# Kernel optimization log

Hardware: AMD Instinct MI355X
Metric: run time of the kernel (lower is better)

## Reference

```python
import jax, jax.numpy as jnp
import numpy as np

T, B, E, H = 1024, 4, 1024, 16
D = E // H  # head_dim = 64


def rel_shift(x):
    # Transformer-XL relative shift trick (RelativeShift.forward, batch_first=True).
    # x: [BH, Q, P] -> pad one zero column, reshape [BH, P+1, Q], drop first row, reshape back.
    BH, Q, P = x.shape
    zp = jnp.zeros((BH, Q, 1), x.dtype)
    xp = jnp.concatenate([zp, x], axis=2).reshape(BH, P + 1, Q)
    return xp[:, 1:, :].reshape(BH, Q, P)


def setup_inputs() -> dict:
    key = jax.random.key(0)
    ks = jax.random.split(key, 8)
    std = float(np.sqrt(2.0 / (E + E)))
    causal = jnp.triu(jnp.ones((T, T), dtype=bool), k=1)  # True = masked (future positions)
    return {
        "x": jax.random.normal(ks[0], (T, B, E), dtype=jnp.float32),
        "pos": jax.random.normal(ks[1], (T, 1, E), dtype=jnp.float32),
        "in_proj_weight": jax.random.normal(ks[2], (3 * E, E), dtype=jnp.float32) * std,
        "in_proj_bias": jnp.zeros((3 * E,), dtype=jnp.float32),
        "out_proj_weight": jax.random.normal(ks[3], (E, E), dtype=jnp.float32) * std,
        "out_proj_bias": jnp.zeros((E,), dtype=jnp.float32),
        "pos_proj_weight": jax.random.normal(ks[4], (E, E), dtype=jnp.float32) * std,
        "pos_proj_bias": jnp.zeros((E,), dtype=jnp.float32),
        "r_w_bias": jax.random.normal(ks[5], (H, D), dtype=jnp.float32) * 0.02,
        "r_r_bias": jax.random.normal(ks[6], (H, D), dtype=jnp.float32) * 0.02,
        "attn_mask": causal,
    }


def reference(x, pos, in_proj_weight, in_proj_bias, out_proj_weight, out_proj_bias,
              pos_proj_weight, pos_proj_bias, r_w_bias, r_r_bias, attn_mask):
    Tq, Bb, Ee = x.shape
    scale = 1.0 / np.sqrt(D).astype(np.float32)
    # fused QKV projection; layout [T, B, heads, 3, head_dim] matches
    # view(len_q, bsz*heads, 3, head_dim) in the original.
    qkv = (x @ in_proj_weight.T + in_proj_bias).reshape(Tq, Bb, H, 3, D)
    q = qkv[..., 0, :]  # [T,B,H,D]
    k = qkv[..., 1, :]
    v = qkv[..., 2, :]
    # position projection (shared across batch since pos is [T,1,E])
    r_head_k = (pos[:, 0, :] @ pos_proj_weight.T + pos_proj_bias).reshape(Tq, H, D)  # [P,H,D]
    rw_q = q + r_w_bias  # content bias
    rr_q = q + r_r_bias  # position bias
    ac = jnp.einsum('qbhd,kbhd->bhqk', rw_q, k) * scale            # [B,H,Q,K]
    bd = jnp.einsum('qbhd,phd->bhqp', rr_q, r_head_k) * scale      # [B,H,Q,P]
    bd = rel_shift(bd.reshape(Bb * H, Tq, Tq)).reshape(Bb, H, Tq, Tq)[..., :Tq]
    score = ac + bd
    score = jnp.where(attn_mask[None, None, :, :], -jnp.inf, score)
    attn = jax.nn.softmax(score, axis=-1)                          # [B,H,Q,K]
    ctx = jnp.einsum('bhqk,kbhd->qbhd', attn, v).reshape(Tq, Bb, Ee)
    out = ctx @ out_proj_weight.T + out_proj_bias                  # [T,B,E]
    return out, attn
```

## Files before the change

### kernel.cpp

```cpp
#include <hip/hip_runtime.h>
#include <math.h>

#define TQ 1024
#define BBATCH 4
#define EDIM 1024
#define HHEADS 16
#define DHEAD 64

typedef __bf16 bf16x8 __attribute__((ext_vector_type(8)));
typedef __bf16 bf16x4 __attribute__((ext_vector_type(4)));
typedef float  f32x4  __attribute__((ext_vector_type(4)));

#define LDK 40

template<int MODE>
__global__ __launch_bounds__(256) void gemm_mfma_abt(
    const float* __restrict__ A, const float* __restrict__ B,
    const float* __restrict__ bias, float* __restrict__ C,
    int M, int N, int K)
{
    __shared__ __bf16 As[128 * LDK];
    __shared__ __bf16 Bs[128 * LDK];
    const int tid  = threadIdx.x;
    const int lane = tid & 63;
    const int wid  = tid >> 6;
    const int wr   = wid >> 1, wc = wid & 1;
    const int m0 = blockIdx.y * 128, n0 = blockIdx.x * 128;

    f32x4 acc[4][4] = {};

    const int sm0 = tid >> 2;
    const int sm1 = sm0 + 64;
    const int sk  = (tid & 3) << 3;

    const int fr = lane & 15;
    const int kg = (lane >> 4) << 3;

    for (int k0 = 0; k0 < K; k0 += 32) {
        float4 ra0a = *(const float4*)&A[(size_t)(m0 + sm0) * K + k0 + sk];
        float4 ra0b = *(const float4*)&A[(size_t)(m0 + sm0) * K + k0 + sk + 4];
        float4 ra1a = *(const float4*)&A[(size_t)(m0 + sm1) * K + k0 + sk];
        float4 ra1b = *(const float4*)&A[(size_t)(m0 + sm1) * K + k0 + sk + 4];
        float4 rb0a = *(const float4*)&B[(size_t)(n0 + sm0) * K + k0 + sk];
        float4 rb0b = *(const float4*)&B[(size_t)(n0 + sm0) * K + k0 + sk + 4];
        float4 rb1a = *(const float4*)&B[(size_t)(n0 + sm1) * K + k0 + sk];
        float4 rb1b = *(const float4*)&B[(size_t)(n0 + sm1) * K + k0 + sk + 4];

        __syncthreads();

        bf16x8 w;
        w[0]=(__bf16)ra0a.x; w[1]=(__bf16)ra0a.y; w[2]=(__bf16)ra0a.z; w[3]=(__bf16)ra0a.w;
        w[4]=(__bf16)ra0b.x; w[5]=(__bf16)ra0b.y; w[6]=(__bf16)ra0b.z; w[7]=(__bf16)ra0b.w;
        *(bf16x8*)&As[sm0 * LDK + sk] = w;
        w[0]=(__bf16)ra1a.x; w[1]=(__bf16)ra1a.y; w[2]=(__bf16)ra1a.z; w[3]=(__bf16)ra1a.w;
        w[4]=(__bf16)ra1b.x; w[5]=(__bf16)ra1b.y; w[6]=(__bf16)ra1b.z; w[7]=(__bf16)ra1b.w;
        *(bf16x8*)&As[sm1 * LDK + sk] = w;
        w[0]=(__bf16)rb0a.x; w[1]=(__bf16)rb0a.y; w[2]=(__bf16)rb0a.z; w[3]=(__bf16)rb0a.w;
        w[4]=(__bf16)rb0b.x; w[5]=(__bf16)rb0b.y; w[6]=(__bf16)rb0b.z; w[7]=(__bf16)rb0b.w;
        *(bf16x8*)&Bs[sm0 * LDK + sk] = w;
        w[0]=(__bf16)rb1a.x; w[1]=(__bf16)rb1a.y; w[2]=(__bf16)rb1a.z; w[3]=(__bf16)rb1a.w;
        w[4]=(__bf16)rb1b.x; w[5]=(__bf16)rb1b.y; w[6]=(__bf16)rb1b.z; w[7]=(__bf16)rb1b.w;
        *(bf16x8*)&Bs[sm1 * LDK + sk] = w;

        __syncthreads();

        bf16x8 af[4], bfr[4];
        #pragma unroll
        for (int i = 0; i < 4; ++i) {
            af[i]  = *(const bf16x8*)&As[(wr * 64 + i * 16 + fr) * LDK + kg];
            bfr[i] = *(const bf16x8*)&Bs[(wc * 64 + i * 16 + fr) * LDK + kg];
        }
        #pragma unroll
        for (int mi = 0; mi < 4; ++mi)
        #pragma unroll
        for (int ni = 0; ni < 4; ++ni)
            acc[mi][ni] = __builtin_amdgcn_mfma_f32_16x16x32_bf16(
                af[mi], bfr[ni], acc[mi][ni], 0, 0, 0);
    }

    const int fq = lane >> 4;
    #pragma unroll
    for (int mi = 0; mi < 4; ++mi)
    #pragma unroll
    for (int ni = 0; ni < 4; ++ni) {
        int row = m0 + wr * 64 + mi * 16 + fq * 4;
        int col = n0 + wc * 64 + ni * 16 + fr;
        float bv = bias[col];
        #pragma unroll
        for (int j = 0; j < 4; ++j) {
            float v = acc[mi][ni][j] + bv;
            if (MODE == 0) {
                C[(size_t)(row + j) * N + col] = v;
            } else {
                C[(((size_t)(col >> 6) << 10) + (row + j)) * 64 + (col & 63)] = v;
            }
        }
    }
}

__global__ __launch_bounds__(256) void bias_dots_kernel(
    const float* __restrict__ qkv, const float* __restrict__ Rm,
    const float* __restrict__ rwb, const float* __restrict__ rrb,
    float* __restrict__ cK, float* __restrict__ cR)
{
    int id = blockIdx.x * 256 + threadIdx.x;
    if (id < 65536) {
        int bh = id >> 10, k = id & 1023;
        int b = bh >> 4, h = bh & 15;
        const float* p = &qkv[((size_t)k * 4 + b) * 3072 + h * 192 + 64];
        const float* w = &rwb[h << 6];
        float s = 0.f;
        #pragma unroll
        for (int d = 0; d < 64; d += 4) {
            float4 v = *(const float4*)&p[d];
            s += v.x * w[d] + v.y * w[d + 1] + v.z * w[d + 2] + v.w * w[d + 3];
        }
        cK[id] = s;
    } else if (id < 81920) {
        int id2 = id - 65536;
        int h = id2 >> 10, j = id2 & 1023;
        const float* p = &Rm[(((size_t)h << 10) + j) * 64];
        const float* w = &rrb[h << 6];
        float s = 0.f;
        #pragma unroll
        for (int d = 0; d < 64; d += 4) {
            float4 v = *(const float4*)&p[d];
            s += v.x * w[d] + v.y * w[d + 1] + v.z * w[d + 2] + v.w * w[d + 3];
        }
        cR[id2] = s;
    }
}

#define SLD 72

__global__ __launch_bounds__(256) void score_mfma_kernel(
    const float* __restrict__ qkv, const float* __restrict__ Rm,
    const float* __restrict__ cK, const float* __restrict__ cR,
    float* __restrict__ attn)
{
    int t = blockIdx.x;
    int qt = (int)((sqrtf(8.f * t + 1.f) - 1.f) * 0.5f);
    while ((qt + 1) * (qt + 2) / 2 <= t) ++qt;
    while (qt * (qt + 1) / 2 > t) --qt;
    int kt = t - qt * (qt + 1) / 2;

    const int bh = blockIdx.y;
    const int b = bh >> 4, h = bh & 15;
    const int q0 = qt << 6, k0 = kt << 6;
    const int tid = threadIdx.x, lane = tid & 63, wid = tid >> 6;
    const int fr = lane & 15, fq = lane >> 4, kg = fq << 3;
    const int w16 = wid << 4;
    const int base_j = k0 - q0 + 960;

    __shared__ __bf16 Qs[64 * SLD];
    __shared__ __bf16 Ks[64 * SLD];
    __shared__ __bf16 Rs[64 * SLD];
    __shared__ float  BDs[64][68];

    float4 qreg[4], kreg[4], r0reg[4], r1reg[4];
    #pragma unroll
    for (int s = 0; s < 4; ++s) {
        int idx = (s << 8) + tid;
        int r = idx >> 4, dc = (idx & 15) << 2;
        qreg[s] = *(const float4*)&qkv[((size_t)(q0 + r) * 4 + b) * 3072 + h * 192 + dc];
        kreg[s] = *(const float4*)&qkv[((size_t)(k0 + r) * 4 + b) * 3072 + h * 192 + 64 + dc];
        int j0 = base_j + r;       if (j0 > 1023) j0 = 1023;
        int j1 = base_j + 64 + r;  if (j1 > 1023) j1 = 1023;
        r0reg[s] = *(const float4*)&Rm[(((size_t)h << 10) + j0) * 64 + dc];
        r1reg[s] = *(const float4*)&Rm[(((size_t)h << 10) + j1) * 64 + dc];
    }
    #pragma unroll
    for (int s = 0; s < 4; ++s) {
        int idx = (s << 8) + tid;
        int r = idx >> 4, dc = (idx & 15) << 2;
        bf16x4 w;
        w[0]=(__bf16)qreg[s].x; w[1]=(__bf16)qreg[s].y; w[2]=(__bf16)qreg[s].z; w[3]=(__bf16)qreg[s].w;
        *(bf16x4*)&Qs[r * SLD + dc] = w;
        w[0]=(__bf16)kreg[s].x; w[1]=(__bf16)kreg[s].y; w[2]=(__bf16)kreg[s].z; w[3]=(__bf16)kreg[s].w;
        *(bf16x4*)&Ks[r * SLD + dc] = w;
        w[0]=(__bf16)r0reg[s].x; w[1]=(__bf16)r0reg[s].y; w[2]=(__bf16)r0reg[s].z; w[3]=(__bf16)r0reg[s].w;
        *(bf16x4*)&Rs[r * SLD + dc] = w;
    }
    __syncthreads();

    bf16x8 af0 = *(const bf16x8*)&Qs[(w16 + fr) * SLD + kg];
    bf16x8 af1 = *(const bf16x8*)&Qs[(w16 + fr) * SLD + 32 + kg];

    f32x4 aac[4], abd[4];
    const f32x4 zero4 = {0.f, 0.f, 0.f, 0.f};

    #pragma unroll
    for (int ni = 0; ni < 4; ++ni) {
        bf16x8 b0 = *(const bf16x8*)&Ks[(ni * 16 + fr) * SLD + kg];
        bf16x8 b1 = *(const bf16x8*)&Ks[(ni * 16 + fr) * SLD + 32 + kg];
        aac[ni] = __builtin_amdgcn_mfma_f32_16x16x32_bf16(af0, b0, zero4, 0, 0, 0);
        aac[ni] = __builtin_amdgcn_mfma_f32_16x16x32_bf16(af1, b1, aac[ni], 0, 0, 0);
    }
    #pragma unroll
    for (int ni = 0; ni < 4; ++ni) {
        bf16x8 b0 = *(const bf16x8*)&Rs[(ni * 16 + fr) * SLD + kg];
        bf16x8 b1 = *(const bf16x8*)&Rs[(ni * 16 + fr) * SLD + 32 + kg];
        abd[ni] = __builtin_amdgcn_mfma_f32_16x16x32_bf16(af0, b0, zero4, 0, 0, 0);
        abd[ni] = __builtin_amdgcn_mfma_f32_16x16x32_bf16(af1, b1, abd[ni], 0, 0, 0);
    }
    #pragma unroll
    for (int ni = 0; ni < 4; ++ni)
    #pragma unroll
    for (int j = 0; j < 4; ++j)
        BDs[w16 + fq * 4 + j][ni * 16 + fr] = abd[ni][j];
    asm volatile("s_waitcnt lgkmcnt(0)" ::: "memory");
    #pragma unroll
    for (int ni = 0; ni < 4; ++ni)
    #pragma unroll
    for (int j = 0; j < 4; ++j) {
        int lrow = w16 + fq * 4 + j;
        int widx = (ni * 16 + fr) - lrow + 63;
        if (widx < 64) aac[ni][j] += BDs[lrow][widx];
    }
    __syncthreads();

    #pragma unroll
    for (int s = 0; s < 4; ++s) {
        int idx = (s << 8) + tid;
        int r = idx >> 4, dc = (idx & 15) << 2;
        bf16x4 w;
        w[0]=(__bf16)r1reg[s].x; w[1]=(__bf16)r1reg[s].y; w[2]=(__bf16)r1reg[s].z; w[3]=(__bf16)r1reg[s].w;
        *(bf16x4*)&Rs[r * SLD + dc] = w;
    }
    __syncthreads();

    #pragma unroll
    for (int ni = 0; ni < 4; ++ni) {
        bf16x8 b0 = *(const bf16x8*)&Rs[(ni * 16 + fr) * SLD + kg];
        bf16x8 b1 = *(const bf16x8*)&Rs[(ni * 16 + fr) * SLD + 32 + kg];
        abd[ni] = __builtin_amdgcn_mfma_f32_16x16x32_bf16(af0, b0, zero4, 0, 0, 0);
        abd[ni] = __builtin_amdgcn_mfma_f32_16x16x32_bf16(af1, b1, abd[ni], 0, 0, 0);
    }
    #pragma unroll
    for (int ni = 0; ni < 4; ++ni)
    #pragma unroll
    for (int j = 0; j < 4; ++j)
        BDs[w16 + fq * 4 + j][ni * 16 + fr] = abd[ni][j];
    asm volatile("s_waitcnt lgkmcnt(0)" ::: "memory");
    #pragma unroll
    for (int ni = 0; ni < 4; ++ni)
    #pragma unroll
    for (int j = 0; j < 4; ++j) {
        int lrow = w16 + fq * 4 + j;
        int widx = (ni * 16 + fr) - lrow + 63;
        if (widx >= 64) aac[ni][j] += BDs[lrow][widx - 64];
    }

    #pragma unroll
    for (int ni = 0; ni < 4; ++ni) {
        int lcol = ni * 16 + fr;
        int k = k0 + lcol;
        float ckv = cK[(bh << 10) + k];
        #pragma unroll
        for (int j = 0; j < 4; ++j) {
            int lrow = w16 + fq * 4 + j;
            int q = q0 + lrow;
            int widx = lcol - lrow + 63;
            int jidx = base_j + widx; if (jidx > 1023) jidx = 1023;
            float crv = cR[(h << 10) + jidx];
            float v = 0.125f * (aac[ni][j] + ckv + crv);
            attn[((((size_t)bh << 10) + q) << 10) + k] = v;
        }
    }
}

__global__ __launch_bounds__(256) void softmax_kernel(float* __restrict__ attn)
{
    const int q = blockIdx.x, bh = blockIdx.y;
    float* row = attn + ((((size_t)bh << 10) + q) << 10);
    const int tid = threadIdx.x;
    float4 v = *(const float4*)&row[tid << 2];
    float s[4] = {v.x, v.y, v.z, v.w};
    #pragma unroll
    for (int c = 0; c < 4; ++c)
        if (((tid << 2) + c) > q) s[c] = -INFINITY;

    float m = fmaxf(fmaxf(s[0], s[1]), fmaxf(s[2], s[3]));
    #pragma unroll
    for (int off = 32; off > 0; off >>= 1)
        m = fmaxf(m, __shfl_xor(m, off));
    __shared__ float redm[4];
    __shared__ float reds[4];
    const int lane = tid & 63, wid = tid >> 6;
    if (lane == 0) redm[wid] = m;
    __syncthreads();
    m = fmaxf(fmaxf(redm[0], redm[1]), fmaxf(redm[2], redm[3]));

    float e[4];
    float t = 0.f;
    #pragma unroll
    for (int c = 0; c < 4; ++c) { e[c] = expf(s[c] - m); t += e[c]; }
    #pragma unroll
    for (int off = 32; off > 0; off >>= 1)
        t += __shfl_xor(t, off);
    if (lane == 0) reds[wid] = t;
    __syncthreads();
    t = reds[0] + reds[1] + reds[2] + reds[3];
    float inv = 1.0f / t;
    float4 o;
    o.x = e[0] * inv; o.y = e[1] * inv; o.z = e[2] * inv; o.w = e[3] * inv;
    *(float4*)&row[tid << 2] = o;
}

__global__ __launch_bounds__(256) void ctx_kernel(
    const float* __restrict__ attn, const float* __restrict__ qkv,
    float* __restrict__ ctx)
{
    const int qt = blockIdx.x, bh = blockIdx.y;
    const int b = bh >> 4, h = bh & 15;
    const int q0 = qt << 6;
    const int tid = threadIdx.x, tx = tid & 15, ty = tid >> 4;
    __shared__ __align__(16) float At[64][68];
    __shared__ __align__(16) float Vs[64][68];
    float acc[4][4] = {};

    for (int k0 = 0; k0 <= q0; k0 += 64) {
        #pragma unroll
        for (int s = 0; s < 4; ++s) {
            int idx = s * 256 + tid;
            int r = idx >> 4, cc = (idx & 15) << 2;
            *(float4*)&At[r][cc] =
                *(const float4*)&attn[((((size_t)bh << 10) + q0 + r) << 10) + k0 + cc];
            *(float4*)&Vs[r][cc] =
                *(const float4*)&qkv[((size_t)(k0 + r) * 4 + b) * 3072 + h * 192 + 128 + cc];
        }
        __syncthreads();
        #pragma unroll
        for (int kk = 0; kk < 64; ++kk) {
            float a[4];
            #pragma unroll
            for (int i = 0; i < 4; ++i) a[i] = At[(ty << 2) + i][kk];
            float4 vv = *(const float4*)&Vs[kk][tx << 2];
            float vb[4] = {vv.x, vv.y, vv.z, vv.w};
            #pragma unroll
            for (int i = 0; i < 4; ++i)
            #pragma unroll
            for (int j = 0; j < 4; ++j)
                acc[i][j] += a[i] * vb[j];
        }
        __syncthreads();
    }

    #pragma unroll
    for (int i = 0; i < 4; ++i) {
        int q = q0 + (ty << 2) + i;
        float4 o;
        o.x = acc[i][0]; o.y = acc[i][1]; o.z = acc[i][2]; o.w = acc[i][3];
        *(float4*)&ctx[((size_t)q * 4 + b) * 1024 + (h << 6) + (tx << 2)] = o;
    }
}

extern "C" void kernel_launch(void* const* d_in, const int* in_sizes, int n_in,
                              void* d_out, int out_size, void* d_ws, size_t ws_size,
                              hipStream_t stream)
{
    (void)in_sizes; (void)n_in; (void)out_size; (void)ws_size;
    const float* x     = (const float*)d_in[0];
    const float* pos   = (const float*)d_in[1];
    const float* w_in  = (const float*)d_in[2];
    const float* b_in  = (const float*)d_in[3];
    const float* w_out = (const float*)d_in[4];
    const float* b_out = (const float*)d_in[5];
    const float* w_pos = (const float*)d_in[6];
    const float* b_pos = (const float*)d_in[7];
    const float* rwb   = (const float*)d_in[8];
    const float* rrb   = (const float*)d_in[9];

    float* out  = (float*)d_out;
    float* attn = out + (size_t)TQ * BBATCH * EDIM;

    float* ws  = (float*)d_ws;
    float* qkv = ws;
    float* R   = qkv + (size_t)4096 * 3072;
    float* ctx = R + (size_t)HHEADS * TQ * DHEAD;
    float* cK  = ctx;
    float* cR  = ctx + 65536;

    dim3 blk(256, 1, 1);

    gemm_mfma_abt<0><<<dim3(3072 / 128, 4096 / 128), blk, 0, stream>>>(
        x, w_in, b_in, qkv, 4096, 3072, 1024);
    gemm_mfma_abt<1><<<dim3(1024 / 128, 1024 / 128), blk, 0, stream>>>(
        pos, w_pos, b_pos, R, 1024, 1024, 1024);
    bias_dots_kernel<<<dim3(320), blk, 0, stream>>>(qkv, R, rwb, rrb, cK, cR);
    score_mfma_kernel<<<dim3(136, 64), blk, 0, stream>>>(qkv, R, cK, cR, attn);
    softmax_kernel<<<dim3(1024, 64), blk, 0, stream>>>(attn);
    ctx_kernel<<<dim3(16, 64), blk, 0, stream>>>(attn, qkv, ctx);
    gemm_mfma_abt<0><<<dim3(1024 / 128, 4096 / 128), blk, 0, stream>>>(
        ctx, w_out, b_out, out, 4096, 1024, 1024);
}
```

Before: 434.4 us.

## Fuse score, softmax and context into one online-softmax attention kernel

Replaces the separate score, softmax and context kernels with one kernel per (query tile, batch-head). The kernel computes scores with an online max/sum across key tiles and writes the raw scores. It then reads them back to normalize, writes the probabilities, and does P·V with bf16 MFMA instead of scalar FP32 FMAs. The masked upper tiles are zero-filled inside the kernel. This removes two launches and the separate full-matrix softmax pass, and moves ctx onto matrix cores. In exchange the grid shrinks to 1024 blocks, whose work varies with the query tile and is ordered largest first. Attention still makes a write-read-write round trip, and cK/cR scratch now lives in the output buffer.

After: 546.0 us. 25.7% more time.

```diff
diff --git a/kernel.cpp b/kernel.cpp
--- a/kernel.cpp
+++ b/kernel.cpp
@@ -131,228 +131,228 @@
     }
 }
 
-#define SLD 72
-
-__global__ __launch_bounds__(256) void score_mfma_kernel(
+#define FLD 66
+
+__global__ __launch_bounds__(256) void fused_attn_kernel(
     const float* __restrict__ qkv, const float* __restrict__ Rm,
     const float* __restrict__ cK, const float* __restrict__ cR,
-    float* __restrict__ attn)
+    float* __restrict__ attn, float* __restrict__ ctx)
 {
-    int t = blockIdx.x;
-    int qt = (int)((sqrtf(8.f * t + 1.f) - 1.f) * 0.5f);
-    while ((qt + 1) * (qt + 2) / 2 <= t) ++qt;
-    while (qt * (qt + 1) / 2 > t) --qt;
-    int kt = t - qt * (qt + 1) / 2;
-
+    const int qt = 15 - blockIdx.x;
     const int bh = blockIdx.y;
     const int b = bh >> 4, h = bh & 15;
-    const int q0 = qt << 6, k0 = kt << 6;
+    const int q0 = qt << 6;
     const int tid = threadIdx.x, lane = tid & 63, wid = tid >> 6;
     const int fr = lane & 15, fq = lane >> 4, kg = fq << 3;
     const int w16 = wid << 4;
-    const int base_j = k0 - q0 + 960;
-
-    __shared__ __bf16 Qs[64 * SLD];
-    __shared__ __bf16 Ks[64 * SLD];
-    __shared__ __bf16 Rs[64 * SLD];
-    __shared__ float  BDs[64][68];
-
-    float4 qreg[4], kreg[4], r0reg[4], r1reg[4];
+    const int base0 = 960 - q0;
+
+    __shared__ __align__(16) char smem[42752];
+    __bf16* Qs  = (__bf16*)smem;
+    __bf16* Pl  = (__bf16*)smem;
+    float (*BDs)[68] = (float(*)[68])smem;
+    __bf16* Vt  = (__bf16*)(smem + 8448);
+    __bf16* Ks  = (__bf16*)(smem + 17408);
+    __bf16* Rc0 = (__bf16*)(smem + 25856);
+    __bf16* Rc1 = (__bf16*)(smem + 34304);
+
     #pragma unroll
     for (int s = 0; s < 4; ++s) {
-        int idx = (s << 8) + tid;
-        int r = idx >> 4, dc = (idx & 15) << 2;
-        qreg[s] = *(const float4*)&qkv[((size_t)(q0 + r) * 4 + b) * 3072 + h * 192 + dc];
-        kreg[s] = *(const float4*)&qkv[((size_t)(k0 + r) * 4 + b) * 3072 + h * 192 + 64 + dc];
-        int j0 = base_j + r;       if (j0 > 1023) j0 = 1023;
-        int j1 = base_j + 64 + r;  if (j1 > 1023) j1 = 1023;
-        r0reg[s] = *(const float4*)&Rm[(((size_t)h << 10) + j0) * 64 + dc];
-        r1reg[s] = *(const float4*)&Rm[(((size_t)h << 10) + j1) * 64 + dc];
-    }
-    #pragma unroll
-    for (int s = 0; s < 4; ++s) {
-        int idx = (s << 8) + tid;
-        int r = idx >> 4, dc = (idx & 15) << 2;
+        int idx = (s << 8) + tid, r = idx >> 4, dc = (idx & 15) << 2;
+        float4 vq = *(const float4*)&qkv[((size_t)(q0 + r) * 4 + b) * 3072 + h * 192 + dc];
+        float4 vr = *(const float4*)&Rm[(((size_t)h << 10) + base0 + r) * 64 + dc];
         bf16x4 w;
-        w[0]=(__bf16)qreg[s].x; w[1]=(__bf16)qreg[s].y; w[2]=(__bf16)qreg[s].z; w[3]=(__bf16)qreg[s].w;
-        *(bf16x4*)&Qs[r * SLD + dc] = w;
-        w[0]=(__bf16)kreg[s].x; w[1]=(__bf16)kreg[s].y; w[2]=(__bf16)kreg[s].z; w[3]=(__bf16)kreg[s].w;
-        *(bf16x4*)&Ks[r * SLD + dc] = w;
-        w[0]=(__bf16)r0reg[s].x; w[1]=(__bf16)r0reg[s].y; w[2]=(__bf16)r0reg[s].z; w[3]=(__bf16)r0reg[s].w;
-        *(bf16x4*)&Rs[r * SLD + dc] = w;
+        w[0]=(__bf16)vq.x; w[1]=(__bf16)vq.y; w[2]=(__bf16)vq.z; w[3]=(__bf16)vq.w;
+        *(bf16x4*)&Qs[r * FLD + dc] = w;
+        w[0]=(__bf16)vr.x; w[1]=(__bf16)vr.y; w[2]=(__bf16)vr.z; w[3]=(__bf16)vr.w;
+        *(bf16x4*)&Rc0[r * FLD + dc] = w;
     }
     __syncthreads();
-
-    bf16x8 af0 = *(const bf16x8*)&Qs[(w16 + fr) * SLD + kg];
-    bf16x8 af1 = *(const bf16x8*)&Qs[(w16 + fr) * SLD + 32 + kg];
-
-    f32x4 aac[4], abd[4];
-    const f32x4 zero4 = {0.f, 0.f, 0.f, 0.f};
-
-    #pragma unroll
-    for (int ni = 0; ni < 4; ++ni) {
-        bf16x8 b0 = *(const bf16x8*)&Ks[(ni * 16 + fr) * SLD + kg];
-        bf16x8 b1 = *(const bf16x8*)&Ks[(ni * 16 + fr) * SLD + 32 + kg];
-        aac[ni] = __builtin_amdgcn_mfma_f32_16x16x32_bf16(af0, b0, zero4, 0, 0, 0);
-        aac[ni] = __builtin_amdgcn_mfma_f32_16x16x32_bf16(af1, b1, aac[ni], 0, 0, 0);
-    }
-    #pragma unroll
-    for (int ni = 0; ni < 4; ++ni) {
-        bf16x8 b0 = *(const bf16x8*)&Rs[(ni * 16 + fr) * SLD + kg];
-        bf16x8 b1 = *(const bf16x8*)&Rs[(ni * 16 + fr) * SLD + 32 + kg];
-        abd[ni] = __builtin_amdgcn_mfma_f32_16x16x32_bf16(af0, b0, zero4, 0, 0, 0);
-        abd[ni] = __builtin_amdgcn_mfma_f32_16x16x32_bf16(af1, b1, abd[ni], 0, 0, 0);
+    bf16x8 af0 = *(const bf16x8*)&Qs[(w16 + fr) * FLD + kg];
+    bf16x8 af1 = *(const bf16x8*)&Qs[(w16 + fr) * FLD + 32 + kg];
+
+    float mrow[4] = {-1e30f, -1e30f, -1e30f, -1e30f};
+    float srow[4] = {0.f, 0.f, 0.f, 0.f};
+    const f32x4 z4 = {0.f, 0.f, 0.f, 0.f};
+
+    for (int kt = 0; kt <= qt; ++kt) {
+        const int k0 = kt << 6;
+        __bf16* Rh0 = (kt & 1) ? Rc1 : Rc0;
+        __bf16* Rh1 = (kt & 1) ? Rc0 : Rc1;
+
+        float4 kreg[4], rreg[4];
+        #pragma unroll
+        for (int s = 0; s < 4; ++s) {
+            int idx = (s << 8) + tid, r = idx >> 4, dc = (idx & 15) << 2;
+            kreg[s] = *(const float4*)&qkv[((size_t)(k0 + r) * 4 + b) * 3072 + h * 192 + 64 + dc];
+            int j = base0 + k0 + 64 + r; if (j > 1023) j = 1023;
+            rreg[s] = *(const float4*)&Rm[(((size_t)h << 10) + j) * 64 + dc];
+        }
+        __syncthreads();
+        #pragma unroll
+        for (int s = 0; s < 4; ++s) {
+            int idx = (s << 8) + tid, r = idx >> 4, dc = (idx & 15) << 2;
+            bf16x4 w;
+            w[0]=(__bf16)kreg[s].x; w[1]=(__bf16)kreg[s].y; w[2]=(__bf16)kreg[s].z; w[3]=(__bf16)kreg[s].w;
+            *(bf16x4*)&Ks[r * FLD + dc] = w;
+            w[0]=(__bf16)rreg[s].x; w[1]=(__bf16)rreg[s].y; w[2]=(__bf16)rreg[s].z; w[3]=(__bf16)rreg[s].w;
+            *(bf16x4*)&Rh1[r * FLD + dc] = w;
+        }
+        __syncthreads();
+
+        f32x4 aac[4];
+        #pragma unroll
+        for (int ni = 0; ni < 4; ++ni) {
+            bf16x8 b0 = *(const bf16x8*)&Ks[(ni * 16 + fr) * FLD + kg];
+            bf16x8 b1 = *(const bf16x8*)&Ks[(ni * 16 + fr) * FLD + 32 + kg];
+            aac[ni] = __builtin_amdgcn_mfma_f32_16x16x32_bf16(af0, b0, z4, 0, 0, 0);
+            aac[ni] = __builtin_amdgcn_mfma_f32_16x16x32_bf16(af1, b1, aac[ni], 0, 0, 0);
+        }
+        f32x4 abd[4];
+        #pragma unroll
+        for (int ni = 0; ni < 4; ++ni) {
+            bf16x8 b0 = *(const bf16x8*)&Rh0[(ni * 16 + fr) * FLD + kg];
+            bf16x8 b1 = *(const bf16x8*)&Rh0[(ni * 16 + fr) * FLD + 32 + kg];
+            abd[ni] = __builtin_amdgcn_mfma_f32_16x16x32_bf16(af0, b0, z4, 0, 0, 0);
+            abd[ni] = __builtin_amdgcn_mfma_f32_16x16x32_bf16(af1, b1, abd[ni], 0, 0, 0);
+        }
+        #pragma unroll
+        for (int ni = 0; ni < 4; ++ni)
+        #pragma unroll
+        for (int j = 0; j < 4; ++j)
+            BDs[w16 + fq * 4 + j][ni * 16 + fr] = abd[ni][j];
+        asm volatile("s_waitcnt lgkmcnt(0)" ::: "memory");
+        #pragma unroll
+        for (int ni = 0; ni < 4; ++ni)
+        #pragma unroll
+        for (int j = 0; j < 4; ++j) {
+            int lrow = w16 + fq * 4 + j;
+            int widx = (ni * 16 + fr) - lrow + 63;
+            if (widx < 64) aac[ni][j] += BDs[lrow][widx];
+        }
+        #pragma unroll
+        for (int ni = 0; ni < 4; ++ni) {
+            bf16x8 b0 = *(const bf16x8*)&Rh1[(ni * 16 + fr) * FLD + kg];
+            bf16x8 b1 = *(const bf16x8*)&Rh1[(ni * 16 + fr) * FLD + 32 + kg];
+            abd[ni] = __builtin_amdgcn_mfma_f32_16x16x32_bf16(af0, b0, z4, 0, 0, 0);
+            abd[ni] = __builtin_amdgcn_mfma_f32_16x16x32_bf16(af1, b1, abd[ni], 0, 0, 0);
+        }
+        #pragma unroll
+        for (int ni = 0; ni < 4; ++ni)
+        #pragma unroll
+        for (int j = 0; j < 4; ++j)
+            BDs[w16 + fq * 4 + j][ni * 16 + fr] = abd[ni][j];
+        asm volatile("s_waitcnt lgkmcnt(0)" ::: "memory");
+        #pragma unroll
+        for (int ni = 0; ni < 4; ++ni)
+        #pragma unroll
+        for (int j = 0; j < 4; ++j) {
+            int lrow = w16 + fq * 4 + j;
+            int widx = (ni * 16 + fr) - lrow + 63;
+            if (widx >= 64) aac[ni][j] += BDs[lrow][widx - 64];
+        }
+
+        float sc[4][4];
+        #pragma unroll
+        for (int ni = 0; ni < 4; ++ni) {
+            int lcol = ni * 16 + fr, k = k0 + lcol;
+            float ckv = cK[(bh << 10) + k];
+            #pragma unroll
+            for (int j = 0; j < 4; ++j) {
+                int lrow = w16 + fq * 4 + j;
+                int widx = lcol - lrow + 63;
+                int jidx = base0 + k0 + widx; if (jidx > 1023) jidx = 1023;
+                float v = 0.125f * (aac[ni][j] + ckv + cR[(h << 10) + jidx]);
+                if (kt == qt && lcol > lrow) v = -1e30f;
+                sc[ni][j] = v;
+                attn[((size_t)bh << 20) + ((size_t)(q0 + lrow) << 10) + k] = v;
+            }
+        }
+        #pragma unroll
+        for (int j = 0; j < 4; ++j) {
+            float tmax = fmaxf(fmaxf(sc[0][j], sc[1][j]), fmaxf(sc[2][j], sc[3][j]));
+            tmax = fmaxf(tmax, __shfl_xor(tmax, 1));
+            tmax = fmaxf(tmax, __shfl_xor(tmax, 2));
+            tmax = fmaxf(tmax, __shfl_xor(tmax, 4));
+            tmax = fmaxf(tmax, __shfl_xor(tmax, 8));
+            float mnew = fmaxf(mrow[j], tmax);
+            float ps = __expf(sc[0][j] - mnew) + __expf(sc[1][j] - mnew)
+                     + __expf(sc[2][j] - mnew) + __expf(sc[3][j] - mnew);
+            ps += __shfl_xor(ps, 1); ps += __shfl_xor(ps, 2);
+            ps += __shfl_xor(ps, 4); ps += __shfl_xor(ps, 8);
+            srow[j] = srow[j] * __expf(mrow[j] - mnew) + ps;
+            mrow[j] = mnew;
+        }
+    }
+
+    float inv[4];
+    #pragma unroll
+    for (int j = 0; j < 4; ++j) inv[j] = 1.0f / srow[j];
+
+    asm volatile("s_waitcnt vmcnt(0)" ::: "memory");
+    __syncthreads();
+
+    f32x4 apv[4] = {};
+    for (int kt = 0; kt <= qt; ++kt) {
+        const int k0 = kt << 6;
+        float4 vreg[4];
+        #pragma unroll
+        for (int s = 0; s < 4; ++s) {
+            int idx = (s << 8) + tid, r = idx >> 4, dc = (idx & 15) << 2;
+            vreg[s] = *(const float4*)&qkv[((size_t)(k0 + r) * 4 + b) * 3072 + h * 192 + 128 + dc];
+        }
+        float praw[4][4];
+        #pragma unroll
+        for (int ni = 0; ni < 4; ++ni)
+        #pragma unroll
+        for (int j = 0; j < 4; ++j)
+            praw[ni][j] = attn[((size_t)bh << 20) +
+                               ((size_t)(q0 + w16 + fq * 4 + j) << 10) + k0 + ni * 16 + fr];
+        __syncthreads();
+        #pragma unroll
+        for (int s = 0; s < 4; ++s) {
+            int idx = (s << 8) + tid, r = idx >> 4, dc = (idx & 15) << 2;
+            Vt[(dc + 0) * FLD + r] = (__bf16)vreg[s].x;
+            Vt[(dc + 1) * FLD + r] = (__bf16)vreg[s].y;
+            Vt[(dc + 2) * FLD + r] = (__bf16)vreg[s].z;
+            Vt[(dc + 3) * FLD + r] = (__bf16)vreg[s].w;
+        }
+        #pragma unroll
+        for (int ni = 0; ni < 4; ++ni)
+        #pragma unroll
+        for (int j = 0; j < 4; ++j) {
+            float p = __expf(praw[ni][j] - mrow[j]) * inv[j];
+            attn[((size_t)bh << 20) +
+                 ((size_t)(q0 + w16 + fq * 4 + j) << 10) + k0 + ni * 16 + fr] = p;
+            Pl[(w16 + fq * 4 + j) * FLD + ni * 16 + fr] = (__bf16)p;
+        }
+        __syncthreads();
+        bf16x8 pa0 = *(const bf16x8*)&Pl[(w16 + fr) * FLD + kg];
+        bf16x8 pa1 = *(const bf16x8*)&Pl[(w16 + fr) * FLD + 32 + kg];
+        #pragma unroll
+        for (int ni = 0; ni < 4; ++ni) {
+            bf16x8 bv0 = *(const bf16x8*)&Vt[(ni * 16 + fr) * FLD + kg];
+            bf16x8 bv1 = *(const bf16x8*)&Vt[(ni * 16 + fr) * FLD + 32 + kg];
+            apv[ni] = __builtin_amdgcn_mfma_f32_16x16x32_bf16(pa0, bv0, apv[ni], 0, 0, 0);
+            apv[ni] = __builtin_amdgcn_mfma_f32_16x16x32_bf16(pa1, bv1, apv[ni], 0, 0, 0);
+        }
+    }
+
+    for (int kt = qt + 1; kt < 16; ++kt) {
+        const int k0 = kt << 6;
+        #pragma unroll
+        for (int s = 0; s < 4; ++s) {
+            int idx = (s << 8) + tid, r = idx >> 4, c4 = (idx & 15) << 2;
+            float4 z = {0.f, 0.f, 0.f, 0.f};
+            *(float4*)&attn[((size_t)bh << 20) + ((size_t)(q0 + r) << 10) + k0 + c4] = z;
+        }
     }
     #pragma unroll
     for (int ni = 0; ni < 4; ++ni)
     #pragma unroll
     for (int j = 0; j < 4; ++j)
-        BDs[w16 + fq * 4 + j][ni * 16 + fr] = abd[ni][j];
-    asm volatile("s_waitcnt lgkmcnt(0)" ::: "memory");
-    #pragma unroll
-    for (int ni = 0; ni < 4; ++ni)
-    #pragma unroll
-    for (int j = 0; j < 4; ++j) {
-        int lrow = w16 + fq * 4 + j;
-        int widx = (ni * 16 + fr) - lrow + 63;
-        if (widx < 64) aac[ni][j] += BDs[lrow][widx];
-    }
-    __syncthreads();
-
-    #pragma unroll
-    for (int s = 0; s < 4; ++s) {
-        int idx = (s << 8) + tid;
-        int r = idx >> 4, dc = (idx & 15) << 2;
-        bf16x4 w;
-        w[0]=(__bf16)r1reg[s].x; w[1]=(__bf16)r1reg[s].y; w[2]=(__bf16)r1reg[s].z; w[3]=(__bf16)r1reg[s].w;
-        *(bf16x4*)&Rs[r * SLD + dc] = w;
-    }
-    __syncthreads();
-
-    #pragma unroll
-    for (int ni = 0; ni < 4; ++ni) {
-        bf16x8 b0 = *(const bf16x8*)&Rs[(ni * 16 + fr) * SLD + kg];
-        bf16x8 b1 = *(const bf16x8*)&Rs[(ni * 16 + fr) * SLD + 32 + kg];
-        abd[ni] = __builtin_amdgcn_mfma_f32_16x16x32_bf16(af0, b0, zero4, 0, 0, 0);
-        abd[ni] = __builtin_amdgcn_mfma_f32_16x16x32_bf16(af1, b1, abd[ni], 0, 0, 0);
-    }
-    #pragma unroll
-    for (int ni = 0; ni < 4; ++ni)
-    #pragma unroll
-    for (int j = 0; j < 4; ++j)
-        BDs[w16 + fq * 4 + j][ni * 16 + fr] = abd[ni][j];
-    asm volatile("s_waitcnt lgkmcnt(0)" ::: "memory");
-    #pragma unroll
-    for (int ni = 0; ni < 4; ++ni)
-    #pragma unroll
-    for (int j = 0; j < 4; ++j) {
-        int lrow = w16 + fq * 4 + j;
-        int widx = (ni * 16 + fr) - lrow + 63;
-        if (widx >= 64) aac[ni][j] += BDs[lrow][widx - 64];
-    }
-
-    #pragma unroll
-    for (int ni = 0; ni < 4; ++ni) {
-        int lcol = ni * 16 + fr;
-        int k = k0 + lcol;
-        float ckv = cK[(bh << 10) + k];
-        #pragma unroll
-        for (int j = 0; j < 4; ++j) {
-            int lrow = w16 + fq * 4 + j;
-            int q = q0 + lrow;
-            int widx = lcol - lrow + 63;
-            int jidx = base_j + widx; if (jidx > 1023) jidx = 1023;
-            float crv = cR[(h << 10) + jidx];
-            float v = 0.125f * (aac[ni][j] + ckv + crv);
-            attn[((((size_t)bh << 10) + q) << 10) + k] = v;
-        }
-    }
-}
-
-__global__ __launch_bounds__(256) void softmax_kernel(float* __restrict__ attn)
-{
-    const int q = blockIdx.x, bh = blockIdx.y;
-    float* row = attn + ((((size_t)bh << 10) + q) << 10);
-    const int tid = threadIdx.x;
-    float4 v = *(const float4*)&row[tid << 2];
-    float s[4] = {v.x, v.y, v.z, v.w};
-    #pragma unroll
-    for (int c = 0; c < 4; ++c)
-        if (((tid << 2) + c) > q) s[c] = -INFINITY;
-
-    float m = fmaxf(fmaxf(s[0], s[1]), fmaxf(s[2], s[3]));
-    #pragma unroll
-    for (int off = 32; off > 0; off >>= 1)
-        m = fmaxf(m, __shfl_xor(m, off));
-    __shared__ float redm[4];
-    __shared__ float reds[4];
-    const int lane = tid & 63, wid = tid >> 6;
-    if (lane == 0) redm[wid] = m;
-    __syncthreads();
-    m = fmaxf(fmaxf(redm[0], redm[1]), fmaxf(redm[2], redm[3]));
-
-    float e[4];
-    float t = 0.f;
-    #pragma unroll
-    for (int c = 0; c < 4; ++c) { e[c] = expf(s[c] - m); t += e[c]; }
-    #pragma unroll
-    for (int off = 32; off > 0; off >>= 1)
-        t += __shfl_xor(t, off);
-    if (lane == 0) reds[wid] = t;
-    __syncthreads();
-    t = reds[0] + reds[1] + reds[2] + reds[3];
-    float inv = 1.0f / t;
-    float4 o;
-    o.x = e[0] * inv; o.y = e[1] * inv; o.z = e[2] * inv; o.w = e[3] * inv;
-    *(float4*)&row[tid << 2] = o;
-}
-
-__global__ __launch_bounds__(256) void ctx_kernel(
-    const float* __restrict__ attn, const float* __restrict__ qkv,
-    float* __restrict__ ctx)
-{
-    const int qt = blockIdx.x, bh = blockIdx.y;
-    const int b = bh >> 4, h = bh & 15;
-    const int q0 = qt << 6;
-    const int tid = threadIdx.x, tx = tid & 15, ty = tid >> 4;
-    __shared__ __align__(16) float At[64][68];
-    __shared__ __align__(16) float Vs[64][68];
-    float acc[4][4] = {};
-
-    for (int k0 = 0; k0 <= q0; k0 += 64) {
-        #pragma unroll
-        for (int s = 0; s < 4; ++s) {
-            int idx = s * 256 + tid;
-            int r = idx >> 4, cc = (idx & 15) << 2;
-            *(float4*)&At[r][cc] =
-                *(const float4*)&attn[((((size_t)bh << 10) + q0 + r) << 10) + k0 + cc];
-            *(float4*)&Vs[r][cc] =
-                *(const float4*)&qkv[((size_t)(k0 + r) * 4 + b) * 3072 + h * 192 + 128 + cc];
-        }
-        __syncthreads();
-        #pragma unroll
-        for (int kk = 0; kk < 64; ++kk) {
-            float a[4];
-            #pragma unroll
-            for (int i = 0; i < 4; ++i) a[i] = At[(ty << 2) + i][kk];
-            float4 vv = *(const float4*)&Vs[kk][tx << 2];
-            float vb[4] = {vv.x, vv.y, vv.z, vv.w};
-            #pragma unroll
-            for (int i = 0; i < 4; ++i)
-            #pragma unroll
-            for (int j = 0; j < 4; ++j)
-                acc[i][j] += a[i] * vb[j];
-        }
-        __syncthreads();
-    }
-
-    #pragma unroll
-    for (int i = 0; i < 4; ++i) {
-        int q = q0 + (ty << 2) + i;
-        float4 o;
-        o.x = acc[i][0]; o.y = acc[i][1]; o.z = acc[i][2]; o.w = acc[i][3];
-        *(float4*)&ctx[((size_t)q * 4 + b) * 1024 + (h << 6) + (tx << 2)] = o;
-    }
+        ctx[((size_t)(q0 + w16 + fq * 4 + j) * 4 + b) * 1024 + (h << 6) + ni * 16 + fr]
+            = apv[ni][j];
 }
 
 extern "C" void kernel_launch(void* const* d_in, const int* in_sizes, int n_in,
@@ -378,8 +378,8 @@
     float* qkv = ws;
     float* R   = qkv + (size_t)4096 * 3072;
     float* ctx = R + (size_t)HHEADS * TQ * DHEAD;
-    float* cK  = ctx;
-    float* cR  = ctx + 65536;
+    float* cK  = out;
+    float* cR  = out + 65536;
 
     dim3 blk(256, 1, 1);
 
@@ -388,9 +388,7 @@
     gemm_mfma_abt<1><<<dim3(1024 / 128, 1024 / 128), blk, 0, stream>>>(
         pos, w_pos, b_pos, R, 1024, 1024, 1024);
     bias_dots_kernel<<<dim3(320), blk, 0, stream>>>(qkv, R, rwb, rrb, cK, cR);
-    score_mfma_kernel<<<dim3(136, 64), blk, 0, stream>>>(qkv, R, cK, cR, attn);
-    softmax_kernel<<<dim3(1024, 64), blk, 0, stream>>>(attn);
-    ctx_kernel<<<dim3(16, 64), blk, 0, stream>>>(attn, qkv, ctx);
+    fused_attn_kernel<<<dim3(16, 64), blk, 0, stream>>>(qkv, R, cK, cR, attn, ctx);
     gemm_mfma_abt<0><<<dim3(1024 / 128, 4096 / 128), blk, 0, stream>>>(
         ctx, w_out, b_out, out, 4096, 1024, 1024);
 }
```

## Split softmax into row-stats pass and fuse normalization into bf16 MFMA PV kernel

Applied to the files above, without the earlier changes.

Replaces the full-row softmax kernel with a per-row statistics kernel that computes an online max and inverse sum while reading only the causal prefix of each row. The context kernel now applies exp and normalization on the fly, writes normalized probabilities back to attn, zero-fills the masked upper tiles, and computes P·V with bf16 MFMA instead of fp32 FMA. The aim is to cut one full read/write pass over the attention matrix, skip reading masked tiles, and use matrix cores. The cost is bf16 rounding in the context product, and scratch stats are placed in the output buffer before the final GEMM overwrites it.

Result: faster. 371.8 us (-14.4%).

```diff
diff --git a/kernel.cpp b/kernel.cpp
--- a/kernel.cpp
+++ b/kernel.cpp
@@ -264,95 +264,132 @@
             int jidx = base_j + widx; if (jidx > 1023) jidx = 1023;
             float crv = cR[(h << 10) + jidx];
             float v = 0.125f * (aac[ni][j] + ckv + crv);
+            if (kt == qt && lcol > lrow) v = -1e30f;
             attn[((((size_t)bh << 10) + q) << 10) + k] = v;
         }
     }
 }
 
-__global__ __launch_bounds__(256) void softmax_kernel(float* __restrict__ attn)
-{
-    const int q = blockIdx.x, bh = blockIdx.y;
-    float* row = attn + ((((size_t)bh << 10) + q) << 10);
-    const int tid = threadIdx.x;
-    float4 v = *(const float4*)&row[tid << 2];
-    float s[4] = {v.x, v.y, v.z, v.w};
-    #pragma unroll
-    for (int c = 0; c < 4; ++c)
-        if (((tid << 2) + c) > q) s[c] = -INFINITY;
-
-    float m = fmaxf(fmaxf(s[0], s[1]), fmaxf(s[2], s[3]));
-    #pragma unroll
-    for (int off = 32; off > 0; off >>= 1)
-        m = fmaxf(m, __shfl_xor(m, off));
-    __shared__ float redm[4];
-    __shared__ float reds[4];
-    const int lane = tid & 63, wid = tid >> 6;
-    if (lane == 0) redm[wid] = m;
-    __syncthreads();
-    m = fmaxf(fmaxf(redm[0], redm[1]), fmaxf(redm[2], redm[3]));
-
-    float e[4];
-    float t = 0.f;
-    #pragma unroll
-    for (int c = 0; c < 4; ++c) { e[c] = expf(s[c] - m); t += e[c]; }
-    #pragma unroll
-    for (int off = 32; off > 0; off >>= 1)
-        t += __shfl_xor(t, off);
-    if (lane == 0) reds[wid] = t;
-    __syncthreads();
-    t = reds[0] + reds[1] + reds[2] + reds[3];
-    float inv = 1.0f / t;
-    float4 o;
-    o.x = e[0] * inv; o.y = e[1] * inv; o.z = e[2] * inv; o.w = e[3] * inv;
-    *(float4*)&row[tid << 2] = o;
-}
-
-__global__ __launch_bounds__(256) void ctx_kernel(
-    const float* __restrict__ attn, const float* __restrict__ qkv,
-    float* __restrict__ ctx)
-{
-    const int qt = blockIdx.x, bh = blockIdx.y;
+__global__ __launch_bounds__(256) void row_stats_kernel(
+    const float* __restrict__ attn, float2* __restrict__ stats)
+{
+    const int gw = blockIdx.x * 4 + (threadIdx.x >> 6);
+    const int bh = gw >> 10, q = gw & 1023;
+    const int lane = threadIdx.x & 63;
+    const float* row = attn + ((size_t)bh << 20) + ((size_t)q << 10);
+
+    float m = -1e30f, s = 0.f;
+    const int nc = (q >> 8) + 1;
+    for (int c = 0; c < nc; ++c) {
+        int base = (c << 8) + (lane << 2);
+        float4 v = *(const float4*)&row[base];
+        bool c0 = base + 0 <= q, c1 = base + 1 <= q, c2 = base + 2 <= q, c3 = base + 3 <= q;
+        float e0 = c0 ? v.x : -1e30f, e1 = c1 ? v.y : -1e30f;
+        float e2 = c2 ? v.z : -1e30f, e3 = c3 ? v.w : -1e30f;
+        float tm = fmaxf(fmaxf(e0, e1), fmaxf(e2, e3));
+        float mn = fmaxf(m, tm);
+        s *= __expf(m - mn);
+        if (c0) s += __expf(v.x - mn);
+        if (c1) s += __expf(v.y - mn);
+        if (c2) s += __expf(v.z - mn);
+        if (c3) s += __expf(v.w - mn);
+        m = mn;
+    }
+    #pragma unroll
+    for (int off = 1; off < 64; off <<= 1) {
+        float mo = __shfl_xor(m, off), so = __shfl_xor(s, off);
+        float mn = fmaxf(m, mo);
+        s = s * __expf(m - mn) + so * __expf(mo - mn);
+        m = mn;
+    }
+    if (lane == 0) stats[gw] = make_float2(m, 1.0f / s);
+}
+
+#define FLD 66
+
+__global__ __launch_bounds__(256) void ctx_norm_kernel(
+    const float* __restrict__ qkv, const float2* __restrict__ stats,
+    float* __restrict__ attn, float* __restrict__ ctx)
+{
+    const int qt = 15 - blockIdx.x;
+    const int bh = blockIdx.y;
     const int b = bh >> 4, h = bh & 15;
     const int q0 = qt << 6;
-    const int tid = threadIdx.x, tx = tid & 15, ty = tid >> 4;
-    __shared__ __align__(16) float At[64][68];
-    __shared__ __align__(16) float Vs[64][68];
-    float acc[4][4] = {};
-
-    for (int k0 = 0; k0 <= q0; k0 += 64) {
+    const int tid = threadIdx.x, lane = tid & 63, wid = tid >> 6;
+    const int fr = lane & 15, fq = lane >> 4, kg = fq << 3;
+    const int w16 = wid << 4;
+
+    __shared__ __bf16 Pl[64 * FLD];
+    __shared__ __bf16 Vt[64 * FLD];
+
+    float mrow[4], inv[4];
+    #pragma unroll
+    for (int j = 0; j < 4; ++j) {
+        float2 st = stats[(bh << 10) + q0 + w16 + fq * 4 + j];
+        mrow[j] = st.x; inv[j] = st.y;
+    }
+
+    f32x4 apv[4] = {};
+    for (int kt = 0; kt <= qt; ++kt) {
+        const int k0 = kt << 6;
+        float4 vreg[4];
         #pragma unroll
         for (int s = 0; s < 4; ++s) {
-            int idx = s * 256 + tid;
-            int r = idx >> 4, cc = (idx & 15) << 2;
-            *(float4*)&At[r][cc] =
-                *(const float4*)&attn[((((size_t)bh << 10) + q0 + r) << 10) + k0 + cc];
-            *(float4*)&Vs[r][cc] =
-                *(const float4*)&qkv[((size_t)(k0 + r) * 4 + b) * 3072 + h * 192 + 128 + cc];
-        }
+            int idx = (s << 8) + tid, r = idx >> 4, dc = (idx & 15) << 2;
+            vreg[s] = *(const float4*)&qkv[((size_t)(k0 + r) * 4 + b) * 3072 + h * 192 + 128 + dc];
+        }
+        float praw[4][4];
+        #pragma unroll
+        for (int ni = 0; ni < 4; ++ni)
+        #pragma unroll
+        for (int j = 0; j < 4; ++j)
+            praw[ni][j] = attn[((size_t)bh << 20) +
+                               ((size_t)(q0 + w16 + fq * 4 + j) << 10) + k0 + ni * 16 + fr];
         __syncthreads();
         #pragma unroll
-        for (int kk = 0; kk < 64; ++kk) {
-            float a[4];
-            #pragma unroll
-            for (int i = 0; i < 4; ++i) a[i] = At[(ty << 2) + i][kk];
-            float4 vv = *(const float4*)&Vs[kk][tx << 2];
-            float vb[4] = {vv.x, vv.y, vv.z, vv.w};
-            #pragma unroll
-            for (int i = 0; i < 4; ++i)
-            #pragma unroll
-            for (int j = 0; j < 4; ++j)
-                acc[i][j] += a[i] * vb[j];
+        for (int s = 0; s < 4; ++s) {
+            int idx = (s << 8) + tid, r = idx >> 4, dc = (idx & 15) << 2;
+            Vt[(dc + 0) * FLD + r] = (__bf16)vreg[s].x;
+            Vt[(dc + 1) * FLD + r] = (__bf16)vreg[s].y;
+            Vt[(dc + 2) * FLD + r] = (__bf16)vreg[s].z;
+            Vt[(dc + 3) * FLD + r] = (__bf16)vreg[s].w;
+        }
+        #pragma unroll
+        for (int ni = 0; ni < 4; ++ni)
+        #pragma unroll
+        for (int j = 0; j < 4; ++j) {
+            float p = __expf(praw[ni][j] - mrow[j]) * inv[j];
+            attn[((size_t)bh << 20) +
+                 ((size_t)(q0 + w16 + fq * 4 + j) << 10) + k0 + ni * 16 + fr] = p;
+            Pl[(w16 + fq * 4 + j) * FLD + ni * 16 + fr] = (__bf16)p;
         }
         __syncthreads();
-    }
-
-    #pragma unroll
-    for (int i = 0; i < 4; ++i) {
-        int q = q0 + (ty << 2) + i;
-        float4 o;
-        o.x = acc[i][0]; o.y = acc[i][1]; o.z = acc[i][2]; o.w = acc[i][3];
-        *(float4*)&ctx[((size_t)q * 4 + b) * 1024 + (h << 6) + (tx << 2)] = o;
-    }
+        bf16x8 pa0 = *(const bf16x8*)&Pl[(w16 + fr) * FLD + kg];
+        bf16x8 pa1 = *(const bf16x8*)&Pl[(w16 + fr) * FLD + 32 + kg];
+        #pragma unroll
+        for (int ni = 0; ni < 4; ++ni) {
+            bf16x8 bv0 = *(const bf16x8*)&Vt[(ni * 16 + fr) * FLD + kg];
+            bf16x8 bv1 = *(const bf16x8*)&Vt[(ni * 16 + fr) * FLD + 32 + kg];
+            apv[ni] = __builtin_amdgcn_mfma_f32_16x16x32_bf16(pa0, bv0, apv[ni], 0, 0, 0);
+            apv[ni] = __builtin_amdgcn_mfma_f32_16x16x32_bf16(pa1, bv1, apv[ni], 0, 0, 0);
+        }
+    }
+
+    for (int kt = qt + 1; kt < 16; ++kt) {
+        const int k0 = kt << 6;
+        #pragma unroll
+        for (int s = 0; s < 4; ++s) {
+            int idx = (s << 8) + tid, r = idx >> 4, c4 = (idx & 15) << 2;
+            float4 z = {0.f, 0.f, 0.f, 0.f};
+            *(float4*)&attn[((size_t)bh << 20) + ((size_t)(q0 + r) << 10) + k0 + c4] = z;
+        }
+    }
+    #pragma unroll
+    for (int ni = 0; ni < 4; ++ni)
+    #pragma unroll
+    for (int j = 0; j < 4; ++j)
+        ctx[((size_t)(q0 + w16 + fq * 4 + j) * 4 + b) * 1024 + (h << 6) + ni * 16 + fr]
+            = apv[ni][j];
 }
 
 extern "C" void kernel_launch(void* const* d_in, const int* in_sizes, int n_in,
@@ -378,8 +415,9 @@
     float* qkv = ws;
     float* R   = qkv + (size_t)4096 * 3072;
     float* ctx = R + (size_t)HHEADS * TQ * DHEAD;
-    float* cK  = ctx;
-    float* cR  = ctx + 65536;
+    float*  cK    = out;
+    float*  cR    = out + 65536;
+    float2* stats = (float2*)(out + 81920);
 
     dim3 blk(256, 1, 1);
 
@@ -389,8 +427,8 @@
         pos, w_pos, b_pos, R, 1024, 1024, 1024);
     bias_dots_kernel<<<dim3(320), blk, 0, stream>>>(qkv, R, rwb, rrb, cK, cR);
     score_mfma_kernel<<<dim3(136, 64), blk, 0, stream>>>(qkv, R, cK, cR, attn);
-    softmax_kernel<<<dim3(1024, 64), blk, 0, stream>>>(attn);
-    ctx_kernel<<<dim3(16, 64), blk, 0, stream>>>(attn, qkv, ctx);
+    row_stats_kernel<<<dim3(16384), blk, 0, stream>>>(attn, stats);
+    ctx_norm_kernel<<<dim3(16, 64), blk, 0, stream>>>(qkv, stats, attn, ctx);
     gemm_mfma_abt<0><<<dim3(1024 / 128, 4096 / 128), blk, 0, stream>>>(
         ctx, w_out, b_out, out, 4096, 1024, 1024);
 }
```
